# Performance work log

Measured on AMD Instinct MI355X. Metric: run time of the kernel, lower is better.

The kernel has to match this reference:

```python
import jax, jax.numpy as jnp
import numpy as np
from jax.ops import segment_sum

N_NODES = 100000


def gcn_conv(x, edge_index, W, b, n_nodes):
    # PyG GCNConv: add self-loops, symmetric normalization, linear, scatter-add, bias
    src = jnp.concatenate([edge_index[0], jnp.arange(n_nodes, dtype=edge_index.dtype)])
    dst = jnp.concatenate([edge_index[1], jnp.arange(n_nodes, dtype=edge_index.dtype)])
    deg = segment_sum(jnp.ones(src.shape[0], dtype=x.dtype), dst, num_segments=n_nodes)
    dinv = jnp.where(deg > 0, jax.lax.rsqrt(deg), 0.0)
    norm = dinv[src] * dinv[dst]            # [E+N]
    h = x @ W                               # [N, out] dense GEMM first (PyG order)
    msg = h[src] * norm[:, None]            # gather + scale, [E+N, out]
    out = segment_sum(msg, dst, num_segments=n_nodes)  # scatter-add
    return out + b


def setup_inputs() -> dict:
    key = jax.random.key(0)
    k1, k2, k3, k4, k5, k6 = jax.random.split(key, 6)
    in_c, hid_c, out_c = 128, 128, 64
    n_edges = 1600000
    x = jax.random.normal(k1, (N_NODES, in_c), dtype=jnp.float32)
    edge_index = jax.random.randint(k2, (2, n_edges), 0, N_NODES, dtype=jnp.int64)
    # Glorot-ish init for weights, zeros for bias (PyG defaults)
    W1 = jax.random.normal(k3, (in_c, hid_c), dtype=jnp.float32) / np.sqrt(in_c)
    b1 = jnp.zeros((hid_c,), dtype=jnp.float32)
    W2 = jax.random.normal(k4, (hid_c, out_c), dtype=jnp.float32) / np.sqrt(hid_c)
    b2 = jnp.zeros((out_c,), dtype=jnp.float32)
    return {"x": x, "edge_index": edge_index, "W1": W1, "b1": b1, "W2": W2, "b2": b2}


def reference(x, edge_index, W1, b1, W2, b2):
    h = gcn_conv(x, edge_index, W1, b1, N_NODES)
    h = jax.nn.relu(h)
    out = gcn_conv(h, edge_index, W2, b2, N_NODES)
    return out
```

## Files before the change

### kernel.cpp

```cpp
#include <hip/hip_runtime.h>
#include <hip/hip_fp16.h>

#define NN 100000
#define NBKT 196
#define BCAP 16384

using f16x8 = __attribute__((ext_vector_type(8))) _Float16;
using f32x4 = __attribute__((ext_vector_type(4))) float;

__device__ __forceinline__ void fma4(float4& a, float s, const float4& w) {
  a.x = fmaf(s, w.x, a.x);
  a.y = fmaf(s, w.y, a.y);
  a.z = fmaf(s, w.z, a.z);
  a.w = fmaf(s, w.w, a.w);
}

__device__ __forceinline__ void acc8(float* a, float w, uint4 q) {
  const __half2* p = (const __half2*)&q;
#pragma unroll
  for (int j = 0; j < 4; ++j) {
    float2 f = __half22float2(p[j]);
    a[2 * j]     = fmaf(w, f.x, a[2 * j]);
    a[2 * j + 1] = fmaf(w, f.y, a[2 * j + 1]);
  }
}

__device__ __forceinline__ unsigned packh2(float x, float y) {
  __half2 h = __floats2half2_rn(x, y);
  return *(unsigned*)&h;
}

__global__ void k_detect(const int* __restrict__ e, int* flag, int E) {
  if (threadIdx.x == 0 && blockIdx.x == 0) {
    int n = E < 64 ? E : 64;
    int m = 1;
    for (int i = 0; i < n; ++i) {
      if (e[2 * i + 1] != 0) { m = 0; break; }
    }
    *flag = m;
  }
}

__global__ void k_gcur_init(int* __restrict__ gcur) {
  int b = blockIdx.x * 256 + threadIdx.x;
  if (b < NBKT) gcur[b] = b * BCAP;
}

__global__ __launch_bounds__(256) void k_binA(const int* __restrict__ e,
                                              const int* __restrict__ flag,
                                              int* __restrict__ gcur,
                                              unsigned int* __restrict__ tmp, int E) {
  __shared__ int cnt[256];
  __shared__ int pcur[256];
  const int tid = threadIdx.x;
  const int start = blockIdx.x * 4096;
  const int m = *flag;
  cnt[tid] = 0;
  __syncthreads();
  int ss[16], dd[16];
#pragma unroll
  for (int k = 0; k < 16; ++k) {
    int i = start + tid + k * 256;
    int s = -1, d = 0;
    if (i < E) {
      if (m) { s = e[2 * i]; d = e[2 * (E + i)]; }
      else   { s = e[i];     d = e[E + i]; }
      atomicAdd(&cnt[d >> 9], 1);
    }
    ss[k] = s; dd[k] = d;
  }
  __syncthreads();
  if (tid < NBKT && cnt[tid] > 0) pcur[tid] = atomicAdd(&gcur[tid], cnt[tid]);
  __syncthreads();
#pragma unroll
  for (int k = 0; k < 16; ++k) {
    if (ss[k] >= 0) {
      int b = dd[k] >> 9;
      int p = atomicAdd(&pcur[b], 1);
      tmp[p] = ((unsigned)ss[k] << 9) | (unsigned)(dd[k] & 511);
    }
  }
}

__global__ __launch_bounds__(256) void k_bkt_scan(const int* __restrict__ gcur,
                                                  int* __restrict__ bktbase,
                                                  int* __restrict__ rowptr) {
  __shared__ int s[256];
  const int tid = threadIdx.x;
  int v = (tid < NBKT) ? (gcur[tid] - tid * BCAP) : 0;
  s[tid] = v;
  __syncthreads();
#pragma unroll
  for (int off = 1; off < 256; off <<= 1) {
    int t = (tid >= off) ? s[tid - off] : 0;
    __syncthreads();
    s[tid] += t;
    __syncthreads();
  }
  if (tid < NBKT) bktbase[tid] = s[tid] - v;
  if (tid == 255) {
    bktbase[NBKT] = s[255];
    rowptr[NN] = s[255];
  }
}

__global__ __launch_bounds__(256) void k_binB(const unsigned int* __restrict__ tmp,
                                              const int* __restrict__ gcur,
                                              const int* __restrict__ bktbase,
                                              int* __restrict__ rowptr,
                                              float* __restrict__ dinv,
                                              int* __restrict__ srcs) {
  __shared__ int hist[512];
  __shared__ int lofs[512];
  __shared__ int sbuf[256];
  const int b = blockIdx.x;
  const int tid = threadIdx.x;
  const int tbeg = b * BCAP;
  const int tend = gcur[b];
  const int base = bktbase[b];
  hist[tid] = 0;
  hist[tid + 256] = 0;
  __syncthreads();
  for (int j = tbeg + tid; j < tend; j += 256) atomicAdd(&hist[tmp[j] & 511], 1);
  __syncthreads();
  int a0 = hist[2 * tid], a1 = hist[2 * tid + 1];
  int sv = a0 + a1;
  sbuf[tid] = sv;
  __syncthreads();
#pragma unroll
  for (int off = 1; off < 256; off <<= 1) {
    int t = (tid >= off) ? sbuf[tid - off] : 0;
    __syncthreads();
    sbuf[tid] += t;
    __syncthreads();
  }
  int excl = sbuf[tid] - sv;
  lofs[2 * tid] = excl;
  lofs[2 * tid + 1] = excl + a0;
  __syncthreads();
  for (int i = tid; i < 512; i += 256) {
    int node = (b << 9) + i;
    if (node < NN) {
      rowptr[node] = base + lofs[i];
      dinv[node] = rsqrtf((float)(hist[i] + 1));
    }
  }
  __syncthreads();
  for (int j = tbeg + tid; j < tend; j += 256) {
    unsigned v = tmp[j];
    int p = base + atomicAdd(&lofs[v & 511], 1);
    srcs[p] = (int)(v >> 9);
  }
}

template <int N>
__global__ void k_wt(const float* __restrict__ W, _Float16* __restrict__ Wt) {
  int i = blockIdx.x * 256 + threadIdx.x;
  if (i >= 128 * N) return;
  int n = i >> 7, k = i & 127;
  Wt[i] = (_Float16)W[k * N + n];
}

template <int N, bool RELU, bool AHALF>
__global__ __launch_bounds__(256) void k_gemm_mfma(const void* __restrict__ Av,
                                                   const _Float16* __restrict__ Wt,
                                                   _Float16* __restrict__ out, int M) {
  constexpr int NF = N / 16;
  __shared__ _Float16 As[64 * 136];
  __shared__ _Float16 Bs[N * 136];
  const int tid = threadIdx.x;
  const long long row0 = (long long)blockIdx.x * 64;
  if (AHALF) {
    const _Float16* A = (const _Float16*)Av;
#pragma unroll
    for (int t = 0; t < 4; ++t) {
      int i = tid + t * 256;
      int m = i >> 4, q = i & 15;
      long long row = row0 + m;
      uint4 v = make_uint4(0, 0, 0, 0);
      if (row < M) v = ((const uint4*)A)[row * 16 + q];
      if (RELU) {
        unsigned* pw = (unsigned*)&v;
#pragma unroll
        for (int j = 0; j < 4; ++j) {
          unsigned u = pw[j];
          unsigned lo = (u & 0x8000u) ? 0u : (u & 0xffffu);
          unsigned hi = (u & 0x80000000u) ? 0u : (u & 0xffff0000u);
          pw[j] = lo | hi;
        }
      }
      *(uint4*)&As[m * 136 + q * 8] = v;
    }
  } else {
    const float* A = (const float*)Av;
#pragma unroll
    for (int t = 0; t < 8; ++t) {
      int i = tid + t * 256;
      int m = i >> 5, q = i & 31;
      long long row = row0 + m;
      float4 v = make_float4(0.f, 0.f, 0.f, 0.f);
      if (row < M) v = ((const float4*)A)[row * 32 + q];
      if (RELU) {
        v.x = fmaxf(v.x, 0.f); v.y = fmaxf(v.y, 0.f);
        v.z = fmaxf(v.z, 0.f); v.w = fmaxf(v.w, 0.f);
      }
      uint2 w2 = make_uint2(packh2(v.x, v.y), packh2(v.z, v.w));
      *(uint2*)&As[m * 136 + q * 4] = w2;
    }
  }
#pragma unroll
  for (int t = 0; t < N / 16; ++t) {
    int i = tid + t * 256;
    int n = i >> 4, q = i & 15;
    uint4 v = ((const uint4*)Wt)[i];
    *(uint4*)&Bs[n * 136 + q * 8] = v;
  }
  __syncthreads();
  const int lane = tid & 63;
  const int wrow = (tid >> 6) * 16;
  const int r = lane & 15, g = lane >> 4;
  f32x4 acc[NF] = {};
#pragma unroll
  for (int ks = 0; ks < 4; ++ks) {
    f16x8 av = *(const f16x8*)&As[(wrow + r) * 136 + ks * 32 + g * 8];
#pragma unroll
    for (int cf = 0; cf < NF; ++cf) {
      f16x8 bv = *(const f16x8*)&Bs[(cf * 16 + r) * 136 + ks * 32 + g * 8];
      acc[cf] = __builtin_amdgcn_mfma_f32_16x16x32_f16(av, bv, acc[cf], 0, 0, 0);
    }
  }
#pragma unroll
  for (int cf = 0; cf < NF; ++cf) {
#pragma unroll
    for (int q = 0; q < 4; ++q) {
      long long row = row0 + wrow + g * 4 + q;
      if (row < M) out[row * N + cf * 16 + r] = (_Float16)acc[cf][q];
    }
  }
}

template <int C, bool HOUT>
__global__ __launch_bounds__(256) void k_gather_h(const int* __restrict__ rowptr,
                                                  const int* __restrict__ srcs,
                                                  const float* __restrict__ dinv,
                                                  const _Float16* __restrict__ h,
                                                  const float* __restrict__ b,
                                                  void* __restrict__ outv) {
  constexpr int LPN = C / 8;
  constexpr int NPW = 64 / LPN;
  constexpr int NPB = NPW * 4;
  const int wave = threadIdx.x >> 6;
  const int lane = threadIdx.x & 63;
  const int grp = lane / LPN;
  const int li = lane % LPN;
  const int node = blockIdx.x * NPB + wave * NPW + grp;
  if (node >= NN) return;
  const float dd = dinv[node];
  float acc[8];
  {
    uint4 q = *(const uint4*)(h + (long long)node * C + li * 8);
    const __half2* p = (const __half2*)&q;
#pragma unroll
    for (int j = 0; j < 4; ++j) {
      float2 f = __half22float2(p[j]);
      acc[2 * j]     = dd * f.x;
      acc[2 * j + 1] = dd * f.y;
    }
  }
  const int beg = rowptr[node], end = rowptr[node + 1];
  int e = beg;
  for (; e + 2 <= end; e += 2) {
    int s0 = srcs[e], s1 = srcs[e + 1];
    float w0 = dinv[s0], w1 = dinv[s1];
    uint4 q0 = *(const uint4*)(h + (long long)s0 * C + li * 8);
    uint4 q1 = *(const uint4*)(h + (long long)s1 * C + li * 8);
    acc8(acc, w0, q0);
    acc8(acc, w1, q1);
  }
  if (e < end) {
    int s0 = srcs[e];
    float w0 = dinv[s0];
    uint4 q0 = *(const uint4*)(h + (long long)s0 * C + li * 8);
    acc8(acc, w0, q0);
  }
  const float4* b4 = (const float4*)b;
  float4 bb0 = b4[li * 2], bb1 = b4[li * 2 + 1];
  float o[8];
  o[0] = fmaf(dd, acc[0], bb0.x);
  o[1] = fmaf(dd, acc[1], bb0.y);
  o[2] = fmaf(dd, acc[2], bb0.z);
  o[3] = fmaf(dd, acc[3], bb0.w);
  o[4] = fmaf(dd, acc[4], bb1.x);
  o[5] = fmaf(dd, acc[5], bb1.y);
  o[6] = fmaf(dd, acc[6], bb1.z);
  o[7] = fmaf(dd, acc[7], bb1.w);
  if (HOUT) {
    uint4 w;
    w.x = packh2(o[0], o[1]);
    w.y = packh2(o[2], o[3]);
    w.z = packh2(o[4], o[5]);
    w.w = packh2(o[6], o[7]);
    *(uint4*)((_Float16*)outv + (long long)node * C + li * 8) = w;
  } else {
    float4* op = (float4*)((float*)outv + (long long)node * C + li * 8);
    op[0] = make_float4(o[0], o[1], o[2], o[3]);
    op[1] = make_float4(o[4], o[5], o[6], o[7]);
  }
}

__global__ void k_zero_i32(int* p, int n) {
  int i = blockIdx.x * 256 + threadIdx.x;
  if (i < n) p[i] = 0;
}

__global__ void k_deg_count(const int* __restrict__ e, const int* __restrict__ flag,
                            int* __restrict__ deg, int E) {
  int i = blockIdx.x * 256 + threadIdx.x;
  if (i >= E) return;
  int m = *flag;
  int d = m ? e[2 * (E + i)] : e[E + i];
  atomicAdd(&deg[d], 1);
}

__global__ void k_dinv_f(const int* __restrict__ deg, float* __restrict__ dinv) {
  int i = blockIdx.x * 256 + threadIdx.x;
  if (i < NN) dinv[i] = rsqrtf((float)(deg[i] + 1));
}

template <int N, bool RELU>
__global__ __launch_bounds__(256) void k_gemm_v(const float* __restrict__ A,
                                                const float* __restrict__ W,
                                                float* __restrict__ out, int M) {
  constexpr int K4 = 32;
  constexpr int N4 = N / 4;
  constexpr int CG = N4;
  constexpr int ROWS = (256 / CG) * 4;
  __shared__ float4 Wl[128 * N4];
  __shared__ float4 Xl[ROWS * K4];
  const int tid = threadIdx.x;
  const float4* W4 = (const float4*)W;
  for (int i = tid; i < 128 * N4; i += 256) Wl[i] = W4[i];
  const long long row0 = (long long)blockIdx.x * ROWS;
  const float4* A4 = (const float4*)A;
  for (int i = tid; i < ROWS * K4; i += 256) {
    int r = i >> 5;
    long long row = row0 + r;
    float4 v = make_float4(0.f, 0.f, 0.f, 0.f);
    if (row < M) v = A4[row * K4 + (i & 31)];
    if (RELU) {
      v.x = fmaxf(v.x, 0.f); v.y = fmaxf(v.y, 0.f);
      v.z = fmaxf(v.z, 0.f); v.w = fmaxf(v.w, 0.f);
    }
    Xl[i] = v;
  }
  __syncthreads();
  const int c = tid % CG;
  const int rb = (tid / CG) * 4;
  float4 a0 = make_float4(0, 0, 0, 0), a1 = a0, a2 = a0, a3 = a0;
#pragma unroll 4
  for (int k4 = 0; k4 < K4; ++k4) {
    float4 w0 = Wl[(k4 * 4 + 0) * N4 + c];
    float4 w1 = Wl[(k4 * 4 + 1) * N4 + c];
    float4 w2 = Wl[(k4 * 4 + 2) * N4 + c];
    float4 w3 = Wl[(k4 * 4 + 3) * N4 + c];
    float4 x0 = Xl[(rb + 0) * K4 + k4];
    float4 x1 = Xl[(rb + 1) * K4 + k4];
    float4 x2 = Xl[(rb + 2) * K4 + k4];
    float4 x3 = Xl[(rb + 3) * K4 + k4];
    fma4(a0, x0.x, w0); fma4(a0, x0.y, w1); fma4(a0, x0.z, w2); fma4(a0, x0.w, w3);
    fma4(a1, x1.x, w0); fma4(a1, x1.y, w1); fma4(a1, x1.z, w2); fma4(a1, x1.w, w3);
    fma4(a2, x2.x, w0); fma4(a2, x2.y, w1); fma4(a2, x2.z, w2); fma4(a2, x2.w, w3);
    fma4(a3, x3.x, w0); fma4(a3, x3.y, w1); fma4(a3, x3.z, w2); fma4(a3, x3.w, w3);
  }
  float4* O4 = (float4*)out;
  long long row = row0 + rb;
  if (row + 0 < M) O4[(row + 0) * N4 + c] = a0;
  if (row + 1 < M) O4[(row + 1) * N4 + c] = a1;
  if (row + 2 < M) O4[(row + 2) * N4 + c] = a2;
  if (row + 3 < M) O4[(row + 3) * N4 + c] = a3;
}

template <int C>
__global__ void k_self_bias(const float* __restrict__ h, const float* __restrict__ dinv,
                            const float* __restrict__ b, float* __restrict__ out) {
  constexpr int C4 = C / 4;
  int gid = blockIdx.x * 256 + threadIdx.x;
  if (gid >= NN * C4) return;
  int node = gid / C4;
  int cq = gid % C4;
  float di = dinv[node];
  float sc = di * di;
  float4 v = ((const float4*)h)[gid];
  float4 bb = ((const float4*)b)[cq];
  float4 o;
  o.x = fmaf(v.x, sc, bb.x);
  o.y = fmaf(v.y, sc, bb.y);
  o.z = fmaf(v.z, sc, bb.z);
  o.w = fmaf(v.w, sc, bb.w);
  ((float4*)out)[gid] = o;
}

template <int C>
__global__ void k_scatter(const int* __restrict__ e, const int* __restrict__ flag,
                          const float* __restrict__ dinv, const float* __restrict__ h,
                          float* __restrict__ out, int E) {
  constexpr int TPE = C / 4;
  long long gid = (long long)blockIdx.x * blockDim.x + threadIdx.x;
  int ei = (int)(gid / TPE);
  int cq = (int)(gid % TPE);
  if (ei >= E) return;
  int m = *flag;
  int s, d;
  if (m) { s = e[2 * ei]; d = e[2 * (E + ei)]; }
  else   { s = e[ei];     d = e[E + ei]; }
  float nrm = dinv[s] * dinv[d];
  float4 v = ((const float4*)h)[(long long)s * TPE + cq];
  float* op = out + (long long)d * C + (long long)cq * 4;
  unsafeAtomicAdd(op + 0, v.x * nrm);
  unsafeAtomicAdd(op + 1, v.y * nrm);
  unsafeAtomicAdd(op + 2, v.z * nrm);
  unsafeAtomicAdd(op + 3, v.w * nrm);
}

extern "C" void kernel_launch(void* const* d_in, const int* in_sizes, int n_in,
                              void* d_out, int out_size, void* d_ws, size_t ws_size,
                              hipStream_t stream) {
  const float* x  = (const float*)d_in[0];
  const int*   e  = (const int*)d_in[1];
  const float* W1 = (const float*)d_in[2];
  const float* b1 = (const float*)d_in[3];
  const float* W2 = (const float*)d_in[4];
  const float* b2 = (const float*)d_in[5];
  float* out = (float*)d_out;
  const int E = in_sizes[1] / 2;

  char* ws = (char*)d_ws;
  const size_t o_flag    = 0;
  const size_t o_dinv    = 16;
  const size_t o_rowptr  = 400016;
  const size_t o_gcur    = 800032;
  const size_t o_bktbase = 800832;
  const size_t o_tmp     = 801632;
  const size_t o_srcs    = 13646688;
  const size_t o_wt1     = 20046688;
  const size_t o_wt2     = 20079456;
  const size_t o_h       = 20095840;
  const size_t o_out1    = 45695840;
  const size_t need_csr  = 71295840;

  int*      flag    = (int*)(ws + o_flag);
  float*    dinv    = (float*)(ws + o_dinv);
  int*      rowptr  = (int*)(ws + o_rowptr);
  int*      gcur    = (int*)(ws + o_gcur);
  int*      bktbase = (int*)(ws + o_bktbase);
  unsigned* tmp     = (unsigned*)(ws + o_tmp);
  int*      srcs    = (int*)(ws + o_srcs);
  _Float16* wt1     = (_Float16*)(ws + o_wt1);
  _Float16* wt2     = (_Float16*)(ws + o_wt2);
  _Float16* hh      = (_Float16*)(ws + o_h);
  _Float16* out1    = (_Float16*)(ws + o_out1);

  k_detect<<<1, 64, 0, stream>>>(e, flag, E);

  if (ws_size >= need_csr) {
    k_gcur_init<<<1, 256, 0, stream>>>(gcur);
    k_wt<128><<<64, 256, 0, stream>>>(W1, wt1);
    k_wt<64><<<32, 256, 0, stream>>>(W2, wt2);
    k_binA<<<(E + 4095) / 4096, 256, 0, stream>>>(e, flag, gcur, tmp, E);
    k_bkt_scan<<<1, 256, 0, stream>>>(gcur, bktbase, rowptr);
    k_binB<<<NBKT, 256, 0, stream>>>(tmp, gcur, bktbase, rowptr, dinv, srcs);

    k_gemm_mfma<128, false, false><<<(NN + 63) / 64, 256, 0, stream>>>(x, wt1, hh, NN);
    k_gather_h<128, true><<<(NN + 15) / 16, 256, 0, stream>>>(rowptr, srcs, dinv, hh, b1, out1);

    k_gemm_mfma<64, true, true><<<(NN + 63) / 64, 256, 0, stream>>>(out1, wt2, hh, NN);
    k_gather_h<64, false><<<(NN + 31) / 32, 256, 0, stream>>>(rowptr, srcs, dinv, hh, b2, out);
  } else {
    int*   deg   = (int*)(ws + 400016);
    float* hF    = (float*)(ws + (1 << 20));
    float* out1F = (float*)(ws + (1 << 20) + 51200000);
    k_zero_i32<<<(NN + 255) / 256, 256, 0, stream>>>(deg, NN);
    k_deg_count<<<(E + 255) / 256, 256, 0, stream>>>(e, flag, deg, E);
    k_dinv_f<<<(NN + 255) / 256, 256, 0, stream>>>(deg, dinv);
    k_gemm_v<128, false><<<(NN + 31) / 32, 256, 0, stream>>>(x, W1, hF, NN);
    k_self_bias<128><<<(NN * 32 + 255) / 256, 256, 0, stream>>>(hF, dinv, b1, out1F);
    long long tot1 = (long long)E * 32;
    k_scatter<128><<<(int)((tot1 + 255) / 256), 256, 0, stream>>>(e, flag, dinv, hF, out1F, E);
    k_gemm_v<64, true><<<(NN + 63) / 64, 256, 0, stream>>>(out1F, W2, hF, NN);
    k_self_bias<64><<<(NN * 16 + 255) / 256, 256, 0, stream>>>(hF, dinv, b2, out);
    long long tot2 = (long long)E * 16;
    k_scatter<64><<<(int)((tot2 + 255) / 256), 256, 0, stream>>>(e, flag, dinv, hF, out, E);
  }
}
```

Measured before the change: 234.5 us.

## Fold source-side normalization into GEMM epilogue and merge prep kernels

```diff
diff --git a/kernel.cpp b/kernel.cpp
--- a/kernel.cpp
+++ b/kernel.cpp
@@ -15,13 +15,13 @@
   a.w = fmaf(s, w.w, a.w);
 }
 
-__device__ __forceinline__ void acc8(float* a, float w, uint4 q) {
+__device__ __forceinline__ void add8(float* a, uint4 q) {
   const __half2* p = (const __half2*)&q;
 #pragma unroll
   for (int j = 0; j < 4; ++j) {
     float2 f = __half22float2(p[j]);
-    a[2 * j]     = fmaf(w, f.x, a[2 * j]);
-    a[2 * j + 1] = fmaf(w, f.y, a[2 * j + 1]);
+    a[2 * j]     += f.x;
+    a[2 * j + 1] += f.y;
   }
 }
 
@@ -30,20 +30,33 @@
   return *(unsigned*)&h;
 }
 
-__global__ void k_detect(const int* __restrict__ e, int* flag, int E) {
-  if (threadIdx.x == 0 && blockIdx.x == 0) {
-    int n = E < 64 ? E : 64;
-    int m = 1;
-    for (int i = 0; i < n; ++i) {
-      if (e[2 * i + 1] != 0) { m = 0; break; }
-    }
-    *flag = m;
-  }
-}
-
-__global__ void k_gcur_init(int* __restrict__ gcur) {
-  int b = blockIdx.x * 256 + threadIdx.x;
-  if (b < NBKT) gcur[b] = b * BCAP;
+__global__ __launch_bounds__(256) void k_prep(const float* __restrict__ W1,
+                                              const float* __restrict__ W2,
+                                              _Float16* __restrict__ wt1,
+                                              _Float16* __restrict__ wt2,
+                                              int* __restrict__ gcur,
+                                              const int* __restrict__ e,
+                                              int* __restrict__ flag, int E) {
+  const int b = blockIdx.x;
+  const int tid = threadIdx.x;
+  if (b < 64) {
+    int i = b * 256 + tid;
+    int n = i >> 7, k = i & 127;
+    wt1[i] = (_Float16)W1[k * 128 + n];
+  } else if (b < 96) {
+    int i = (b - 64) * 256 + tid;
+    int n = i >> 7, k = i & 127;
+    wt2[i] = (_Float16)W2[k * 64 + n];
+  } else {
+    if (tid < NBKT) gcur[tid] = tid * BCAP;
+    if (tid == 255) {
+      int n = E < 64 ? E : 64;
+      int m = 1;
+      for (int i = 0; i < n; ++i)
+        if (e[2 * i + 1] != 0) { m = 0; break; }
+      *flag = m;
+    }
+  }
 }
 
 __global__ __launch_bounds__(256) void k_binA(const int* __restrict__ e,
@@ -63,8 +76,13 @@
     int i = start + tid + k * 256;
     int s = -1, d = 0;
     if (i < E) {
-      if (m) { s = e[2 * i]; d = e[2 * (E + i)]; }
-      else   { s = e[i];     d = e[E + i]; }
+      if (m) {
+        s = (int)((const long long*)e)[i];
+        d = (int)((const long long*)e)[E + i];
+      } else {
+        s = e[i];
+        d = e[E + i];
+      }
       atomicAdd(&cnt[d >> 9], 1);
     }
     ss[k] = s; dd[k] = d;
@@ -153,17 +171,10 @@
   }
 }
 
-template <int N>
-__global__ void k_wt(const float* __restrict__ W, _Float16* __restrict__ Wt) {
-  int i = blockIdx.x * 256 + threadIdx.x;
-  if (i >= 128 * N) return;
-  int n = i >> 7, k = i & 127;
-  Wt[i] = (_Float16)W[k * N + n];
-}
-
-template <int N, bool RELU, bool AHALF>
+template <int N, bool AHALF>
 __global__ __launch_bounds__(256) void k_gemm_mfma(const void* __restrict__ Av,
                                                    const _Float16* __restrict__ Wt,
+                                                   const float* __restrict__ dinv,
                                                    _Float16* __restrict__ out, int M) {
   constexpr int NF = N / 16;
   __shared__ _Float16 As[64 * 136];
@@ -179,16 +190,6 @@
       long long row = row0 + m;
       uint4 v = make_uint4(0, 0, 0, 0);
       if (row < M) v = ((const uint4*)A)[row * 16 + q];
-      if (RELU) {
-        unsigned* pw = (unsigned*)&v;
-#pragma unroll
-        for (int j = 0; j < 4; ++j) {
-          unsigned u = pw[j];
-          unsigned lo = (u & 0x8000u) ? 0u : (u & 0xffffu);
-          unsigned hi = (u & 0x80000000u) ? 0u : (u & 0xffff0000u);
-          pw[j] = lo | hi;
-        }
-      }
       *(uint4*)&As[m * 136 + q * 8] = v;
     }
   } else {
@@ -200,10 +201,6 @@
       long long row = row0 + m;
       float4 v = make_float4(0.f, 0.f, 0.f, 0.f);
       if (row < M) v = ((const float4*)A)[row * 32 + q];
-      if (RELU) {
-        v.x = fmaxf(v.x, 0.f); v.y = fmaxf(v.y, 0.f);
-        v.z = fmaxf(v.z, 0.f); v.w = fmaxf(v.w, 0.f);
-      }
       uint2 w2 = make_uint2(packh2(v.x, v.y), packh2(v.z, v.w));
       *(uint2*)&As[m * 136 + q * 4] = w2;
     }
@@ -230,17 +227,19 @@
     }
   }
 #pragma unroll
-  for (int cf = 0; cf < NF; ++cf) {
-#pragma unroll
-    for (int q = 0; q < 4; ++q) {
-      long long row = row0 + wrow + g * 4 + q;
-      if (row < M) out[row * N + cf * 16 + r] = (_Float16)acc[cf][q];
-    }
-  }
-}
-
-template <int C, bool HOUT>
-__global__ __launch_bounds__(256) void k_gather_h(const int* __restrict__ rowptr,
+  for (int q = 0; q < 4; ++q) {
+    long long row = row0 + wrow + g * 4 + q;
+    if (row < M) {
+      float sc = dinv[row];
+#pragma unroll
+      for (int cf = 0; cf < NF; ++cf)
+        out[row * N + cf * 16 + r] = (_Float16)(sc * acc[cf][q]);
+    }
+  }
+}
+
+template <int C, bool RELU16>
+__global__ __launch_bounds__(256) void k_gather_s(const int* __restrict__ rowptr,
                                                   const int* __restrict__ srcs,
                                                   const float* __restrict__ dinv,
                                                   const _Float16* __restrict__ h,
@@ -263,25 +262,26 @@
 #pragma unroll
     for (int j = 0; j < 4; ++j) {
       float2 f = __half22float2(p[j]);
-      acc[2 * j]     = dd * f.x;
-      acc[2 * j + 1] = dd * f.y;
+      acc[2 * j]     = f.x;
+      acc[2 * j + 1] = f.y;
     }
   }
   const int beg = rowptr[node], end = rowptr[node + 1];
   int e = beg;
-  for (; e + 2 <= end; e += 2) {
-    int s0 = srcs[e], s1 = srcs[e + 1];
-    float w0 = dinv[s0], w1 = dinv[s1];
+  for (; e + 4 <= end; e += 4) {
+    int s0 = srcs[e], s1 = srcs[e + 1], s2 = srcs[e + 2], s3 = srcs[e + 3];
     uint4 q0 = *(const uint4*)(h + (long long)s0 * C + li * 8);
     uint4 q1 = *(const uint4*)(h + (long long)s1 * C + li * 8);
-    acc8(acc, w0, q0);
-    acc8(acc, w1, q1);
-  }
-  if (e < end) {
-    int s0 = srcs[e];
-    float w0 = dinv[s0];
-    uint4 q0 = *(const uint4*)(h + (long long)s0 * C + li * 8);
-    acc8(acc, w0, q0);
+    uint4 q2 = *(const uint4*)(h + (long long)s2 * C + li * 8);
+    uint4 q3 = *(const uint4*)(h + (long long)s3 * C + li * 8);
+    add8(acc, q0);
+    add8(acc, q1);
+    add8(acc, q2);
+    add8(acc, q3);
+  }
+  for (; e < end; ++e) {
+    uint4 q0 = *(const uint4*)(h + (long long)srcs[e] * C + li * 8);
+    add8(acc, q0);
   }
   const float4* b4 = (const float4*)b;
   float4 bb0 = b4[li * 2], bb1 = b4[li * 2 + 1];
@@ -294,7 +294,9 @@
   o[5] = fmaf(dd, acc[5], bb1.y);
   o[6] = fmaf(dd, acc[6], bb1.z);
   o[7] = fmaf(dd, acc[7], bb1.w);
-  if (HOUT) {
+  if (RELU16) {
+#pragma unroll
+    for (int j = 0; j < 8; ++j) o[j] = fmaxf(o[j], 0.f);
     uint4 w;
     w.x = packh2(o[0], o[1]);
     w.y = packh2(o[2], o[3]);
@@ -311,6 +313,16 @@
 __global__ void k_zero_i32(int* p, int n) {
   int i = blockIdx.x * 256 + threadIdx.x;
   if (i < n) p[i] = 0;
+}
+
+__global__ void k_detect_f(const int* __restrict__ e, int* flag, int E) {
+  if (threadIdx.x == 0 && blockIdx.x == 0) {
+    int n = E < 64 ? E : 64;
+    int m = 1;
+    for (int i = 0; i < n; ++i)
+      if (e[2 * i + 1] != 0) { m = 0; break; }
+    *flag = m;
+  }
 }
 
 __global__ void k_deg_count(const int* __restrict__ e, const int* __restrict__ flag,
@@ -460,25 +472,22 @@
   _Float16* hh      = (_Float16*)(ws + o_h);
   _Float16* out1    = (_Float16*)(ws + o_out1);
 
-  k_detect<<<1, 64, 0, stream>>>(e, flag, E);
-
   if (ws_size >= need_csr) {
-    k_gcur_init<<<1, 256, 0, stream>>>(gcur);
-    k_wt<128><<<64, 256, 0, stream>>>(W1, wt1);
-    k_wt<64><<<32, 256, 0, stream>>>(W2, wt2);
+    k_prep<<<97, 256, 0, stream>>>(W1, W2, wt1, wt2, gcur, e, flag, E);
     k_binA<<<(E + 4095) / 4096, 256, 0, stream>>>(e, flag, gcur, tmp, E);
     k_bkt_scan<<<1, 256, 0, stream>>>(gcur, bktbase, rowptr);
     k_binB<<<NBKT, 256, 0, stream>>>(tmp, gcur, bktbase, rowptr, dinv, srcs);
 
-    k_gemm_mfma<128, false, false><<<(NN + 63) / 64, 256, 0, stream>>>(x, wt1, hh, NN);
-    k_gather_h<128, true><<<(NN + 15) / 16, 256, 0, stream>>>(rowptr, srcs, dinv, hh, b1, out1);
-
-    k_gemm_mfma<64, true, true><<<(NN + 63) / 64, 256, 0, stream>>>(out1, wt2, hh, NN);
-    k_gather_h<64, false><<<(NN + 31) / 32, 256, 0, stream>>>(rowptr, srcs, dinv, hh, b2, out);
+    k_gemm_mfma<128, false><<<(NN + 63) / 64, 256, 0, stream>>>(x, wt1, dinv, hh, NN);
+    k_gather_s<128, true><<<(NN + 15) / 16, 256, 0, stream>>>(rowptr, srcs, dinv, hh, b1, out1);
+
+    k_gemm_mfma<64, true><<<(NN + 63) / 64, 256, 0, stream>>>(out1, wt2, dinv, hh, NN);
+    k_gather_s<64, false><<<(NN + 31) / 32, 256, 0, stream>>>(rowptr, srcs, dinv, hh, b2, out);
   } else {
     int*   deg   = (int*)(ws + 400016);
     float* hF    = (float*)(ws + (1 << 20));
     float* out1F = (float*)(ws + (1 << 20) + 51200000);
+    k_detect_f<<<1, 64, 0, stream>>>(e, flag, E);
     k_zero_i32<<<(NN + 255) / 256, 256, 0, stream>>>(deg, NN);
     k_deg_count<<<(E + 255) / 256, 256, 0, stream>>>(e, flag, deg, E);
     k_dinv_f<<<(NN + 255) / 256, 256, 0, stream>>>(deg, dinv);
```

Result: faster. 224.2 us (-4.4%).
